# Optimization experiments

Measured on AMD Instinct MI355X. Metric: run time of the kernel, lower is better.

Reference implementation:

```python
import jax, jax.numpy as jnp
import numpy as np

B, EEG_D, FMRI_D, BD, H, NC = 131072, 128, 64, 128, 4, 2
HD = BD // H  # head dim = 32
EPS = 1e-5

def layernorm(x, g, b):
    m = jnp.mean(x, axis=-1, keepdims=True)
    v = jnp.var(x, axis=-1, keepdims=True)
    return (x - m) * jax.lax.rsqrt(v + EPS) * g + b

def setup_inputs() -> dict:
    key = jax.random.key(0)
    ks = jax.random.split(key, 24)
    r = lambda i, shape, s=0.05: jax.random.normal(ks[i], shape, dtype=jnp.float32) * s
    return {
        'eeg_feats': jax.random.normal(ks[0], (B, EEG_D), dtype=jnp.float32),
        'fmri_feats': jax.random.normal(ks[1], (B, FMRI_D), dtype=jnp.float32),
        # projections (weights stored [in, out])
        'We': r(2, (EEG_D, BD)), 'be': jnp.zeros((BD,)),
        'ge': jnp.ones((BD,)), 'bge': jnp.zeros((BD,)),
        'Wf': r(3, (FMRI_D, BD)), 'bf': jnp.zeros((BD,)),
        'gf': jnp.ones((BD,)), 'bgf': jnp.zeros((BD,)),
        # multihead attention
        'Wq': r(4, (BD, BD)), 'bq': jnp.zeros((BD,)),
        'Wk': r(5, (BD, BD)), 'bk': jnp.zeros((BD,)),
        'Wv': r(6, (BD, BD)), 'bv': jnp.zeros((BD,)),
        'Wo': r(7, (BD, BD)), 'bo': jnp.zeros((BD,)),
        # learned fusion
        'fusion_logits': jnp.zeros((2,)),
        'temperature': jnp.ones(()),
        # classifier
        'Wc1': r(8, (BD, BD // 2)), 'bc1': jnp.zeros((BD // 2,)),
        'gc': jnp.ones((BD // 2,)), 'bgc': jnp.zeros((BD // 2,)),
        'Wc2': r(9, (BD // 2, NC)), 'bc2': jnp.zeros((NC,)),
    }

def reference(eeg_feats, fmri_feats, We, be, ge, bge, Wf, bf, gf, bgf,
              Wq, bq, Wk, bk, Wv, bv, Wo, bo, fusion_logits, temperature,
              Wc1, bc1, gc, bgc, Wc2, bc2):
    # modality projections: Linear + LN + GELU (dropout off at eval)
    eeg_p = jax.nn.gelu(layernorm(eeg_feats @ We + be, ge, bge), approximate=False)
    fmri_p = jax.nn.gelu(layernorm(fmri_feats @ Wf + bf, gf, bgf), approximate=False)

    # cross-attention: query = eeg_p (1 token), kv = [eeg_p, fmri_p] (2 tokens)
    seq = jnp.stack([eeg_p, fmri_p], axis=1)                 # [B, 2, BD]
    q = (eeg_p @ Wq + bq).reshape(B, H, HD)                  # [B, H, HD]
    k = (seq @ Wk + bk).reshape(B, 2, H, HD)
    v = (seq @ Wv + bv).reshape(B, 2, H, HD)
    scores = jnp.einsum('bhd,bkhd->bhk', q, k) / jnp.sqrt(jnp.float32(HD))
    attn = jax.nn.softmax(scores, axis=-1)                   # [B, H, 2]
    ctx = jnp.einsum('bhk,bkhd->bhd', attn, v).reshape(B, BD)
    eeg_enh = ctx @ Wo + bo                                  # [B, BD]

    # learned temperature-scaled fusion over [eeg_enhanced, fmri_proj]
    w = jax.nn.softmax(fusion_logits / temperature, axis=0)
    fused = w[0] * eeg_enh + w[1] * fmri_p                   # [B, BD]

    # classifier: Linear + LN + ReLU + Linear
    h = jax.nn.relu(layernorm(fused @ Wc1 + bc1, gc, bgc))
    logits = h @ Wc2 + bc2                                   # [B, NC]
    return logits
```

## Files before the change

### kernel.cpp

```cpp
#include <hip/hip_runtime.h>
#include <math.h>

#define EPS 1e-5f
#define SCALE 0.17677669529663687f

#define OFF_We  0
#define OFF_Wf  16384
#define OFF_Wq  24576
#define OFF_Wk  40960
#define OFF_Wv  57344
#define OFF_Wo  73728
#define OFF_Wc1 90112
#define PACK_TOTAL 98304

#define CHUNK 8192

typedef __bf16 bf16x8 __attribute__((ext_vector_type(8)));
typedef float f32x4 __attribute__((ext_vector_type(4)));
typedef unsigned short ushort_t;
typedef unsigned short ushortx4 __attribute__((ext_vector_type(4)));

__device__ __forceinline__ ushort_t f2bf(float x) {
    unsigned u = __builtin_bit_cast(unsigned, x);
    u = (u + 0x7fffu + ((u >> 16) & 1u)) >> 16;
    return (ushort_t)u;
}
__device__ __forceinline__ float bf2f(ushort_t v) {
    unsigned u = ((unsigned)v) << 16;
    return __builtin_bit_cast(float, u);
}

#define DPPADD(x, ctrl) \
    ((x) + __builtin_bit_cast(float, __builtin_amdgcn_update_dpp( \
        __builtin_bit_cast(int, (x)), __builtin_bit_cast(int, (x)), (ctrl), 0xF, 0xF, false)))

__device__ __forceinline__ float rowsum16(float x) {
    x = DPPADD(x, 0x121);
    x = DPPADD(x, 0x122);
    x = DPPADD(x, 0x124);
    x = DPPADD(x, 0x128);
    return x;
}

__device__ __forceinline__ float gelu_fast(float x) {
    float x2 = x * x;
    float u = x * fmaf(0.07135481283f, x2, 1.5957691216f);
    float e = __expf(-u);
    return x * __builtin_amdgcn_rcpf(1.0f + e);
}

__global__ __launch_bounds__(256) void pack_all(
    const float* __restrict__ We, const float* __restrict__ Wf,
    const float* __restrict__ Wq, const float* __restrict__ Wk,
    const float* __restrict__ Wv, const float* __restrict__ Wo,
    const float* __restrict__ Wc1, ushort_t* __restrict__ ws)
{
    int o = blockIdx.x * 256 + threadIdx.x;
    if (o >= PACK_TOTAL) return;
    const float* W; int K, N, base;
    if (o < OFF_Wf)        { W = We;  K = 128; N = 128; base = OFF_We; }
    else if (o < OFF_Wq)   { W = Wf;  K = 64;  N = 128; base = OFF_Wf; }
    else if (o < OFF_Wk)   { W = Wq;  K = 128; N = 128; base = OFF_Wq; }
    else if (o < OFF_Wv)   { W = Wk;  K = 128; N = 128; base = OFF_Wk; }
    else if (o < OFF_Wo)   { W = Wv;  K = 128; N = 128; base = OFF_Wv; }
    else if (o < OFF_Wc1)  { W = Wo;  K = 128; N = 128; base = OFF_Wo; }
    else                   { W = Wc1; K = 128; N = 64;  base = OFF_Wc1; }
    int e = o - base;
    int j = e & 7, l = (e >> 3) & 63, rest = e >> 9;
    int KS = K >> 5;
    int s = rest % KS, t = rest / KS;
    int k = s * 32 + ((l >> 4) << 3) + j;
    int n = (t << 4) + (l & 15);
    ws[o] = f2bf(W[k * N + n]);
}

template<int KS>
__device__ __forceinline__ void load_af(bf16x8 af[KS], const ushort_t* A, int lane)
{
    const int quad = lane >> 4, l16 = lane & 15;
    #pragma unroll
    for (int ks = 0; ks < KS; ++ks)
        af[ks] = *(const bf16x8*)(A + l16 * 136 + ks * 32 + quad * 8);
}

template<int KS, int NT4>
__device__ __forceinline__ void mma_c(const bf16x8 af[KS], const ushort_t* sW,
                                      f32x4* acc, int lane)
{
    #pragma unroll
    for (int t = 0; t < NT4; ++t)
        #pragma unroll
        for (int ks = 0; ks < KS; ++ks) {
            bf16x8 bb = *(const bf16x8*)(sW + ((t * KS + ks) * 64 + lane) * 8);
            acc[t] = __builtin_amdgcn_mfma_f32_16x16x32_bf16(af[ks], bb, acc[t], 0, 0, 0);
        }
}

__global__ __launch_bounds__(256, 3) void fusion_stage(
    const float* __restrict__ eeg, const float* __restrict__ fmri,
    const float* __restrict__ be, const float* __restrict__ ge, const float* __restrict__ bge,
    const float* __restrict__ bfb, const float* __restrict__ gf, const float* __restrict__ bgf,
    const float* __restrict__ bq, const float* __restrict__ bk, const float* __restrict__ bv,
    const float* __restrict__ bo,
    const float* __restrict__ fusion_logits, const float* __restrict__ temperature,
    const float* __restrict__ bc1, const float* __restrict__ gc, const float* __restrict__ bgc,
    const float* __restrict__ Wc2, const float* __restrict__ bc2,
    const ushort_t* __restrict__ ws, float* __restrict__ out)
{
    __shared__ __align__(16) ushort_t sW[CHUNK];
    __shared__ __align__(16) ushort_t B1[4][16 * 136];
    __shared__ __align__(16) ushort_t B2[4][16 * 136];

    const int tid = threadIdx.x;
    const int wave = tid >> 6, lane = tid & 63;
    const int quad = lane >> 4, l16 = lane & 15;
    const int rowbase = blockIdx.x * 64 + wave * 16;
    ushort_t* b1 = B1[wave];
    ushort_t* b2 = B2[wave];

    auto stageW = [&](int offU) {
        __syncthreads();
        const uint4* g = (const uint4*)(ws + offU);
        uint4* d = (uint4*)sW;
        #pragma unroll
        for (int i = 0; i < 4; ++i) d[tid + i * 256] = g[tid + i * 256];
        __syncthreads();
    };

    {
        const float4* src = (const float4*)(eeg + (size_t)rowbase * 128);
        #pragma unroll
        for (int i = 0; i < 8; ++i) {
            int idx = i * 64 + lane;
            float4 v = src[idx];
            int r = idx >> 5, k4 = (idx & 31) * 4;
            *(ushortx4*)&b1[r * 136 + k4] =
                (ushortx4){f2bf(v.x), f2bf(v.y), f2bf(v.z), f2bf(v.w)};
        }
        const float4* srcf = (const float4*)(fmri + (size_t)rowbase * 64);
        #pragma unroll
        for (int i = 0; i < 4; ++i) {
            int idx = i * 64 + lane;
            float4 v = srcf[idx];
            int r = idx >> 4, k4 = (idx & 15) * 4;
            *(ushortx4*)&b2[r * 136 + k4] =
                (ushortx4){f2bf(v.x), f2bf(v.y), f2bf(v.z), f2bf(v.w)};
        }
    }

    float meanS[4], rstdS[4];

    {
        bf16x8 afR[4]; load_af<4>(afR, b1, lane);
        f32x4 acc[8];
        #pragma unroll
        for (int nt = 0; nt < 8; ++nt) {
            float b = be[nt * 16 + l16];
            acc[nt] = (f32x4){b, b, b, b};
        }
        stageW(OFF_We);          mma_c<4, 4>(afR, sW, acc + 0, lane);
        stageW(OFF_We + CHUNK);  mma_c<4, 4>(afR, sW, acc + 4, lane);
        #pragma unroll
        for (int r = 0; r < 4; ++r) {
            float s = 0.f, ss = 0.f;
            #pragma unroll
            for (int nt = 0; nt < 8; ++nt) { float x = acc[nt][r]; s += x; ss = fmaf(x, x, ss); }
            s = rowsum16(s); ss = rowsum16(ss);
            float m = s * (1.f / 128.f);
            meanS[r] = m;
            rstdS[r] = rsqrtf(ss * (1.f / 128.f) - m * m + EPS);
        }
        #pragma unroll
        for (int nt = 0; nt < 8; ++nt) {
            float g = ge[nt * 16 + l16], bb = bge[nt * 16 + l16];
            #pragma unroll
            for (int r = 0; r < 4; ++r) {
                float x = (acc[nt][r] - meanS[r]) * rstdS[r] * g + bb;
                b1[(quad * 4 + r) * 136 + nt * 16 + l16] = f2bf(gelu_fast(x));
            }
        }
    }

    {
        bf16x8 afR[2]; load_af<2>(afR, b2, lane);
        f32x4 acc[8];
        #pragma unroll
        for (int nt = 0; nt < 8; ++nt) {
            float b = bfb[nt * 16 + l16];
            acc[nt] = (f32x4){b, b, b, b};
        }
        stageW(OFF_Wf);  mma_c<2, 8>(afR, sW, acc, lane);
        #pragma unroll
        for (int r = 0; r < 4; ++r) {
            float s = 0.f, ss = 0.f;
            #pragma unroll
            for (int nt = 0; nt < 8; ++nt) { float x = acc[nt][r]; s += x; ss = fmaf(x, x, ss); }
            s = rowsum16(s); ss = rowsum16(ss);
            float m = s * (1.f / 128.f);
            meanS[r] = m;
            rstdS[r] = rsqrtf(ss * (1.f / 128.f) - m * m + EPS);
        }
        #pragma unroll
        for (int nt = 0; nt < 8; ++nt) {
            float g = gf[nt * 16 + l16], bb = bgf[nt * 16 + l16];
            #pragma unroll
            for (int r = 0; r < 4; ++r) {
                float x = (acc[nt][r] - meanS[r]) * rstdS[r] * g + bb;
                b2[(quad * 4 + r) * 136 + nt * 16 + l16] = f2bf(gelu_fast(x));
            }
        }
    }

    bf16x8 afE[4]; load_af<4>(afE, b1, lane);
    bf16x8 afF[4]; load_af<4>(afF, b2, lane);

    f32x4 q[8];
    {
        #pragma unroll
        for (int nt = 0; nt < 8; ++nt) {
            float b = bq[nt * 16 + l16];
            q[nt] = (f32x4){b, b, b, b};
        }
        stageW(OFF_Wq);          mma_c<4, 4>(afE, sW, q + 0, lane);
        stageW(OFF_Wq + CHUNK);  mma_c<4, 4>(afE, sW, q + 4, lane);
    }

    float a0v[4][4];
    {
        float pd[4][4];
        #pragma unroll
        for (int h = 0; h < 4; ++h)
            #pragma unroll
            for (int r = 0; r < 4; ++r) pd[h][r] = 0.f;
        #pragma unroll
        for (int c = 0; c < 2; ++c) {
            stageW(OFF_Wk + c * CHUNK);
            #pragma unroll
            for (int tl = 0; tl < 4; ++tl) {
                int nt = c * 4 + tl;
                f32x4 e = {0.f, 0.f, 0.f, 0.f}, f = {0.f, 0.f, 0.f, 0.f};
                #pragma unroll
                for (int ks = 0; ks < 4; ++ks) {
                    bf16x8 bb = *(const bf16x8*)(sW + ((tl * 4 + ks) * 64 + lane) * 8);
                    e = __builtin_amdgcn_mfma_f32_16x16x32_bf16(afE[ks], bb, e, 0, 0, 0);
                    f = __builtin_amdgcn_mfma_f32_16x16x32_bf16(afF[ks], bb, f, 0, 0, 0);
                }
                int h = nt >> 1;
                #pragma unroll
                for (int r = 0; r < 4; ++r)
                    pd[h][r] = fmaf(q[nt][r], e[r] - f[r], pd[h][r]);
            }
        }
        #pragma unroll
        for (int h = 0; h < 4; ++h)
            #pragma unroll
            for (int r = 0; r < 4; ++r) {
                float d = rowsum16(pd[h][r]) * SCALE;
                a0v[h][r] = __builtin_amdgcn_rcpf(1.0f + __expf(-d));
            }
    }

    #pragma unroll
    for (int c = 0; c < 2; ++c) {
        stageW(OFF_Wv + c * CHUNK);
        #pragma unroll
        for (int tl = 0; tl < 4; ++tl) {
            int nt = c * 4 + tl;
            float b = bv[nt * 16 + l16];
            f32x4 e = {b, b, b, b}, f = {b, b, b, b};
            #pragma unroll
            for (int ks = 0; ks < 4; ++ks) {
                bf16x8 bb = *(const bf16x8*)(sW + ((tl * 4 + ks) * 64 + lane) * 8);
                e = __builtin_amdgcn_mfma_f32_16x16x32_bf16(afE[ks], bb, e, 0, 0, 0);
                f = __builtin_amdgcn_mfma_f32_16x16x32_bf16(afF[ks], bb, f, 0, 0, 0);
            }
            int h = nt >> 1;
            #pragma unroll
            for (int r = 0; r < 4; ++r) {
                float a0 = a0v[h][r];
                float c0 = a0 * e[r] + (1.0f - a0) * f[r];
                b1[(quad * 4 + r) * 136 + nt * 16 + l16] = f2bf(c0);
            }
        }
    }

    {
        bf16x8 afC[4]; load_af<4>(afC, b1, lane);
        f32x4 acc[8];
        #pragma unroll
        for (int nt = 0; nt < 8; ++nt) {
            float b = bo[nt * 16 + l16];
            acc[nt] = (f32x4){b, b, b, b};
        }
        stageW(OFF_Wo);          mma_c<4, 4>(afC, sW, acc + 0, lane);
        stageW(OFF_Wo + CHUNK);  mma_c<4, 4>(afC, sW, acc + 4, lane);
        float t = temperature[0];
        float dl = (fusion_logits[0] - fusion_logits[1]) / t;
        float w0 = __builtin_amdgcn_rcpf(1.0f + __expf(-dl));
        float w1 = 1.0f - w0;
        #pragma unroll
        for (int nt = 0; nt < 8; ++nt)
            #pragma unroll
            for (int r = 0; r < 4; ++r) {
                int off = (quad * 4 + r) * 136 + nt * 16 + l16;
                float fp = bf2f(b2[off]);
                b1[off] = f2bf(w0 * acc[nt][r] + w1 * fp);
            }
    }

    {
        bf16x8 afU[4]; load_af<4>(afU, b1, lane);
        f32x4 accH[4];
        #pragma unroll
        for (int nt = 0; nt < 4; ++nt) {
            float b = bc1[nt * 16 + l16];
            accH[nt] = (f32x4){b, b, b, b};
        }
        stageW(OFF_Wc1);  mma_c<4, 4>(afU, sW, accH, lane);
        #pragma unroll
        for (int r = 0; r < 4; ++r) {
            float s = 0.f, ss = 0.f;
            #pragma unroll
            for (int nt = 0; nt < 4; ++nt) { float x = accH[nt][r]; s += x; ss = fmaf(x, x, ss); }
            s = rowsum16(s); ss = rowsum16(ss);
            float m = s * (1.f / 64.f);
            meanS[r] = m;
            rstdS[r] = rsqrtf(ss * (1.f / 64.f) - m * m + EPS);
        }
        float hv[4][4];
        #pragma unroll
        for (int nt = 0; nt < 4; ++nt) {
            float g = gc[nt * 16 + l16], bb = bgc[nt * 16 + l16];
            #pragma unroll
            for (int r = 0; r < 4; ++r) {
                float x = (accH[nt][r] - meanS[r]) * rstdS[r] * g + bb;
                hv[nt][r] = fmaxf(x, 0.0f);
            }
        }
        float w2v[4][2];
        #pragma unroll
        for (int nt = 0; nt < 4; ++nt) {
            float2 w = *(const float2*)&Wc2[(nt * 16 + l16) * 2];
            w2v[nt][0] = w.x; w2v[nt][1] = w.y;
        }
        float o0c = bc2[0], o1c = bc2[1];
        #pragma unroll
        for (int r = 0; r < 4; ++r) {
            float p0 = 0.f, p1 = 0.f;
            #pragma unroll
            for (int nt = 0; nt < 4; ++nt) {
                p0 = fmaf(hv[nt][r], w2v[nt][0], p0);
                p1 = fmaf(hv[nt][r], w2v[nt][1], p1);
            }
            p0 = rowsum16(p0); p1 = rowsum16(p1);
            if (l16 == 0) {
                int row = rowbase + quad * 4 + r;
                float2 o; o.x = p0 + o0c; o.y = p1 + o1c;
                *(float2*)&out[row * 2] = o;
            }
        }
    }
}

extern "C" void kernel_launch(void* const* d_in, const int* in_sizes, int n_in,
                              void* d_out, int out_size, void* d_ws, size_t ws_size,
                              hipStream_t stream) {
    const float* eeg  = (const float*)d_in[0];
    const float* fmri = (const float*)d_in[1];
    const float* We   = (const float*)d_in[2];
    const float* be   = (const float*)d_in[3];
    const float* ge   = (const float*)d_in[4];
    const float* bge  = (const float*)d_in[5];
    const float* Wf   = (const float*)d_in[6];
    const float* bf   = (const float*)d_in[7];
    const float* gf   = (const float*)d_in[8];
    const float* bgf  = (const float*)d_in[9];
    const float* Wq   = (const float*)d_in[10];
    const float* bq   = (const float*)d_in[11];
    const float* Wk   = (const float*)d_in[12];
    const float* bk   = (const float*)d_in[13];
    const float* Wv   = (const float*)d_in[14];
    const float* bv   = (const float*)d_in[15];
    const float* Wo   = (const float*)d_in[16];
    const float* bo   = (const float*)d_in[17];
    const float* fl   = (const float*)d_in[18];
    const float* temp = (const float*)d_in[19];
    const float* Wc1  = (const float*)d_in[20];
    const float* bc1  = (const float*)d_in[21];
    const float* gc   = (const float*)d_in[22];
    const float* bgc  = (const float*)d_in[23];
    const float* Wc2  = (const float*)d_in[24];
    const float* bc2  = (const float*)d_in[25];
    float* out = (float*)d_out;
    ushort_t* ws = (ushort_t*)d_ws;

    hipLaunchKernelGGL(pack_all, dim3((PACK_TOTAL + 255) / 256), dim3(256), 0, stream,
                       We, Wf, Wq, Wk, Wv, Wo, Wc1, ws);

    int B = in_sizes[0] / 128;
    int grid = B / 64;
    hipLaunchKernelGGL(fusion_stage, dim3(grid), dim3(256), 0, stream,
                       eeg, fmri, be, ge, bge, bf, gf, bgf,
                       bq, bk, bv, bo, fl, temp, bc1, gc, bgc, Wc2, bc2,
                       ws, out);
}
```

Baseline: 210.7 us.

## Read packed weights directly from global memory instead of staging through LDS

Removes the shared-memory weight staging buffer and its barrier-guarded copy, so each wave loads MFMA B-fragments straight from the prepacked global weight array (relying on L1/L2 caching). This drops about a dozen block-wide __syncthreads and the LDS traffic, lets waves proceed independently, and frees shared memory so launch bounds rise to 4 blocks per CU. The risk is higher global/L2 load latency and traffic per MFMA, since every wave now fetches its own copy of the weights, plus register pressure from the tighter occupancy bound.

```diff
diff --git a/kernel.cpp b/kernel.cpp
--- a/kernel.cpp
+++ b/kernel.cpp
@@ -12,8 +12,6 @@
 #define OFF_Wo  73728
 #define OFF_Wc1 90112
 #define PACK_TOTAL 98304
-
-#define CHUNK 8192
 
 typedef __bf16 bf16x8 __attribute__((ext_vector_type(8)));
 typedef float f32x4 __attribute__((ext_vector_type(4)));
@@ -84,19 +82,19 @@
 }
 
 template<int KS, int NT4>
-__device__ __forceinline__ void mma_c(const bf16x8 af[KS], const ushort_t* sW,
+__device__ __forceinline__ void mma_c(const bf16x8 af[KS], const ushort_t* __restrict__ gW,
                                       f32x4* acc, int lane)
 {
     #pragma unroll
     for (int t = 0; t < NT4; ++t)
         #pragma unroll
         for (int ks = 0; ks < KS; ++ks) {
-            bf16x8 bb = *(const bf16x8*)(sW + ((t * KS + ks) * 64 + lane) * 8);
+            bf16x8 bb = *(const bf16x8*)(gW + ((t * KS + ks) * 64 + lane) * 8);
             acc[t] = __builtin_amdgcn_mfma_f32_16x16x32_bf16(af[ks], bb, acc[t], 0, 0, 0);
         }
 }
 
-__global__ __launch_bounds__(256, 3) void fusion_stage(
+__global__ __launch_bounds__(256, 4) void fusion_stage(
     const float* __restrict__ eeg, const float* __restrict__ fmri,
     const float* __restrict__ be, const float* __restrict__ ge, const float* __restrict__ bge,
     const float* __restrict__ bfb, const float* __restrict__ gf, const float* __restrict__ bgf,
@@ -107,7 +105,6 @@
     const float* __restrict__ Wc2, const float* __restrict__ bc2,
     const ushort_t* __restrict__ ws, float* __restrict__ out)
 {
-    __shared__ __align__(16) ushort_t sW[CHUNK];
     __shared__ __align__(16) ushort_t B1[4][16 * 136];
     __shared__ __align__(16) ushort_t B2[4][16 * 136];
 
@@ -118,15 +115,6 @@
     ushort_t* b1 = B1[wave];
     ushort_t* b2 = B2[wave];
 
-    auto stageW = [&](int offU) {
-        __syncthreads();
-        const uint4* g = (const uint4*)(ws + offU);
-        uint4* d = (uint4*)sW;
-        #pragma unroll
-        for (int i = 0; i < 4; ++i) d[tid + i * 256] = g[tid + i * 256];
-        __syncthreads();
-    };
-
     {
         const float4* src = (const float4*)(eeg + (size_t)rowbase * 128);
         #pragma unroll
@@ -158,8 +146,7 @@
             float b = be[nt * 16 + l16];
             acc[nt] = (f32x4){b, b, b, b};
         }
-        stageW(OFF_We);          mma_c<4, 4>(afR, sW, acc + 0, lane);
-        stageW(OFF_We + CHUNK);  mma_c<4, 4>(afR, sW, acc + 4, lane);
+        mma_c<4, 8>(afR, ws + OFF_We, acc, lane);
         #pragma unroll
         for (int r = 0; r < 4; ++r) {
             float s = 0.f, ss = 0.f;
@@ -189,7 +176,7 @@
             float b = bfb[nt * 16 + l16];
             acc[nt] = (f32x4){b, b, b, b};
         }
-        stageW(OFF_Wf);  mma_c<2, 8>(afR, sW, acc, lane);
+        mma_c<2, 8>(afR, ws + OFF_Wf, acc, lane);
         #pragma unroll
         for (int r = 0; r < 4; ++r) {
             float s = 0.f, ss = 0.f;
@@ -221,8 +208,7 @@
             float b = bq[nt * 16 + l16];
             q[nt] = (f32x4){b, b, b, b};
         }
-        stageW(OFF_Wq);          mma_c<4, 4>(afE, sW, q + 0, lane);
-        stageW(OFF_Wq + CHUNK);  mma_c<4, 4>(afE, sW, q + 4, lane);
+        mma_c<4, 8>(afE, ws + OFF_Wq, q, lane);
     }
 
     float a0v[4][4];
@@ -232,24 +218,20 @@
         for (int h = 0; h < 4; ++h)
             #pragma unroll
             for (int r = 0; r < 4; ++r) pd[h][r] = 0.f;
-        #pragma unroll
-        for (int c = 0; c < 2; ++c) {
-            stageW(OFF_Wk + c * CHUNK);
-            #pragma unroll
-            for (int tl = 0; tl < 4; ++tl) {
-                int nt = c * 4 + tl;
-                f32x4 e = {0.f, 0.f, 0.f, 0.f}, f = {0.f, 0.f, 0.f, 0.f};
-                #pragma unroll
-                for (int ks = 0; ks < 4; ++ks) {
-                    bf16x8 bb = *(const bf16x8*)(sW + ((tl * 4 + ks) * 64 + lane) * 8);
-                    e = __builtin_amdgcn_mfma_f32_16x16x32_bf16(afE[ks], bb, e, 0, 0, 0);
-                    f = __builtin_amdgcn_mfma_f32_16x16x32_bf16(afF[ks], bb, f, 0, 0, 0);
-                }
-                int h = nt >> 1;
-                #pragma unroll
-                for (int r = 0; r < 4; ++r)
-                    pd[h][r] = fmaf(q[nt][r], e[r] - f[r], pd[h][r]);
-            }
+        const ushort_t* gK = ws + OFF_Wk;
+        #pragma unroll
+        for (int nt = 0; nt < 8; ++nt) {
+            f32x4 e = {0.f, 0.f, 0.f, 0.f}, f = {0.f, 0.f, 0.f, 0.f};
+            #pragma unroll
+            for (int ks = 0; ks < 4; ++ks) {
+                bf16x8 bb = *(const bf16x8*)(gK + ((nt * 4 + ks) * 64 + lane) * 8);
+                e = __builtin_amdgcn_mfma_f32_16x16x32_bf16(afE[ks], bb, e, 0, 0, 0);
+                f = __builtin_amdgcn_mfma_f32_16x16x32_bf16(afF[ks], bb, f, 0, 0, 0);
+            }
+            int h = nt >> 1;
+            #pragma unroll
+            for (int r = 0; r < 4; ++r)
+                pd[h][r] = fmaf(q[nt][r], e[r] - f[r], pd[h][r]);
         }
         #pragma unroll
         for (int h = 0; h < 4; ++h)
@@ -260,17 +242,15 @@
             }
     }
 
-    #pragma unroll
-    for (int c = 0; c < 2; ++c) {
-        stageW(OFF_Wv + c * CHUNK);
-        #pragma unroll
-        for (int tl = 0; tl < 4; ++tl) {
-            int nt = c * 4 + tl;
+    {
+        const ushort_t* gV = ws + OFF_Wv;
+        #pragma unroll
+        for (int nt = 0; nt < 8; ++nt) {
             float b = bv[nt * 16 + l16];
             f32x4 e = {b, b, b, b}, f = {b, b, b, b};
             #pragma unroll
             for (int ks = 0; ks < 4; ++ks) {
-                bf16x8 bb = *(const bf16x8*)(sW + ((tl * 4 + ks) * 64 + lane) * 8);
+                bf16x8 bb = *(const bf16x8*)(gV + ((nt * 4 + ks) * 64 + lane) * 8);
                 e = __builtin_amdgcn_mfma_f32_16x16x32_bf16(afE[ks], bb, e, 0, 0, 0);
                 f = __builtin_amdgcn_mfma_f32_16x16x32_bf16(afF[ks], bb, f, 0, 0, 0);
             }
@@ -292,8 +272,7 @@
             float b = bo[nt * 16 + l16];
             acc[nt] = (f32x4){b, b, b, b};
         }
-        stageW(OFF_Wo);          mma_c<4, 4>(afC, sW, acc + 0, lane);
-        stageW(OFF_Wo + CHUNK);  mma_c<4, 4>(afC, sW, acc + 4, lane);
+        mma_c<4, 8>(afC, ws + OFF_Wo, acc, lane);
         float t = temperature[0];
         float dl = (fusion_logits[0] - fusion_logits[1]) / t;
         float w0 = __builtin_amdgcn_rcpf(1.0f + __expf(-dl));
@@ -316,7 +295,7 @@
             float b = bc1[nt * 16 + l16];
             accH[nt] = (f32x4){b, b, b, b};
         }
-        stageW(OFF_Wc1);  mma_c<4, 4>(afU, sW, accH, lane);
+        mma_c<4, 4>(afU, ws + OFF_Wc1, accH, lane);
         #pragma unroll
         for (int r = 0; r < 4; ++r) {
             float s = 0.f, ss = 0.f;
```

Result: slower. 271.4 us (+28.8%).
